# Optimization experiments

Hardware: AMD Instinct MI355X
Metric: run time of the kernel (lower is better)

The kernel has to match this reference:

```python
import jax, jax.numpy as jnp
import numpy as np

MAX_LEN = 200
MAX_K = 3
ITERATION = 3
NEG_PAD = -2.0 ** 16 + 1.0


def setup_inputs() -> dict:
    key = jax.random.key(0)
    k1, k2, k3, k4 = jax.random.split(key, 4)
    B, L, D_in, D_out = 1024, MAX_LEN, 128, 128
    low_capsule = jax.random.normal(k1, (B, L, D_in), dtype=jnp.float32)
    B_matrix = jax.random.normal(k2, (1, MAX_K, L), dtype=jnp.float32)
    S_matrix = jax.random.normal(k3, (D_in, D_out), dtype=jnp.float32)
    # lengths in [1, MAX_LEN]; at least one row hits MAX_LEN so max(seq_len)==MAX_LEN
    seq_len = jax.random.randint(k4, (B, 1), 1, MAX_LEN + 1, dtype=jnp.int64)
    seq_len = seq_len.at[0, 0].set(MAX_LEN)
    return {"low_capsule": low_capsule, "B_matrix": B_matrix,
            "S_matrix": S_matrix, "seq_len": seq_len}


def squash(x):
    # torch code: norm over dim=1 (the capsule axis), keepdim
    sq = jnp.sum(jnp.square(x), axis=1, keepdims=True)
    scale = sq / (1.0 + sq) / jnp.sqrt(sq + 1e-9)
    return scale * x


def reference(low_capsule, B_matrix, S_matrix, seq_len):
    # low_capsule: [B, L, D_in], B_matrix: [1, K, L], S_matrix: [D_in, D_out], seq_len: [B, 1]
    # mask: [B, K, L] (seq_len tiled over K via broadcasting)
    mask = jnp.arange(MAX_LEN)[None, None, :] < seq_len[:, :, None]
    # bilinear projection is loop-invariant (same math as recomputing each iter)
    low_new = jnp.einsum('bld,de->ble', low_capsule, S_matrix)  # [B, L, D_out]
    high = None
    for _ in range(ITERATION):
        logits = jnp.where(mask, B_matrix, jnp.float32(NEG_PAD))  # [B, K, L]
        W = jax.nn.softmax(logits, axis=-1)
        high = squash(jnp.einsum('bkl,ble->bke', W, low_new))  # [B, K, D_out]
        # agreement, summed over batch with keepdim -> [1, K, L]
        B_delta = jnp.einsum('bke,ble->kl', high, low_new)[None]
        B_matrix = B_matrix + B_delta
    return high
```

## Files before the change

kernel.cpp:

```cpp
#include <hip/hip_runtime.h>
#include <math.h>

#define BATCH 1024
#define SEQ   200
#define DIN   128
#define DOUT  128
#define GSTR  260
#define PSTR  608

typedef __attribute__((ext_vector_type(8))) short short8;
typedef __attribute__((ext_vector_type(4))) float f32x4;

__device__ __forceinline__ void async_copy16(const void* g, void* l) {
    __builtin_amdgcn_global_load_lds((const __attribute__((address_space(1))) void*)g,
                                     (__attribute__((address_space(3))) void*)l,
                                     16, 0, 0);
}

__device__ __forceinline__ unsigned pack_split(float f) {
    unsigned u = __float_as_uint(f);
    unsigned r = u + 0x8000u;
    unsigned hi = r >> 16;
    float hf = __uint_as_float(r & 0xffff0000u);
    unsigned lo = __float_as_uint(f - hf) >> 16;
    return (hi << 16) | lo;
}

__device__ __forceinline__ void split2(float f, short& h, short& l) {
    unsigned u = __float_as_uint(f);
    unsigned r = u + 0x8000u;
    h = (short)(r >> 16);
    float hf = __uint_as_float(r & 0xffff0000u);
    l = (short)(__float_as_uint(f - hf) >> 16);
}

__device__ __forceinline__ float unpk(unsigned u) {
    return __uint_as_float(u & 0xffff0000u) + __uint_as_float(u << 16);
}

__global__ __launch_bounds__(256) void k_presplit(const float* __restrict__ S,
                                                  short* __restrict__ Sp) {
    int g = blockIdx.x * 256 + threadIdx.x;
    int j = g & 7, lane = (g >> 3) & 63, kt = (g >> 9) & 3, nt = g >> 11;
    int k = kt * 32 + (lane >> 4) * 8 + j;
    int n = nt * 16 + (lane & 15);
    short h, l;
    split2(S[k * DOUT + n], h, l);
    Sp[g] = h;
    Sp[16384 + g] = l;
}

__global__ __launch_bounds__(256, 4) void k_gemm(const float* __restrict__ A,
                                                 const short* __restrict__ Sp,
                                                 unsigned* __restrict__ outp) {
    __shared__ short sSp[16384];
    const int t = threadIdx.x;
    const int w = t >> 6, lane = t & 63;
    const int q = lane >> 4, c = lane & 15;
    const int cg = blockIdx.x & 1;
    const long rowb = (long)(blockIdx.x >> 1) * 128 + w * 32;

    {
        const int g = w * 4;
#pragma unroll
        for (int i = 0; i < 4; ++i) {
            async_copy16(Sp + cg * 8192 + (g + i) * 512 + lane * 8,
                         &sSp[(g + i) * 512]);
            async_copy16(Sp + 16384 + cg * 8192 + (g + i) * 512 + lane * 8,
                         &sSp[8192 + (g + i) * 512]);
        }
    }

    f32x4 acc[2][4];
    const f32x4 zz = {0.f, 0.f, 0.f, 0.f};
#pragma unroll
    for (int mt = 0; mt < 2; ++mt)
#pragma unroll
        for (int nt = 0; nt < 4; ++nt) acc[mt][nt] = zz;

    float4 buf[2][2][2];
    auto LOADKT = [&](int kt, int p) {
#pragma unroll
        for (int mt = 0; mt < 2; ++mt) {
            const float* ap = A + (rowb + mt * 16 + c) * DIN + kt * 32 + q * 8;
            buf[p][mt][0] = *(const float4*)ap;
            buf[p][mt][1] = *(const float4*)(ap + 4);
        }
    };
    LOADKT(0, 0);
    LOADKT(1, 1);
    __syncthreads();

#pragma unroll
    for (int kt = 0; kt < 4; ++kt) {
        const int p = kt & 1;
        short8 ah[2], al[2];
#pragma unroll
        for (int mt = 0; mt < 2; ++mt) {
            float av[8];
            *(float4*)&av[0] = buf[p][mt][0];
            *(float4*)&av[4] = buf[p][mt][1];
#pragma unroll
            for (int j = 0; j < 8; ++j) {
                short h, l;
                split2(av[j], h, l);
                ah[mt][j] = h; al[mt][j] = l;
            }
        }
        if (kt < 2) LOADKT(kt + 2, p);
#pragma unroll
        for (int nt = 0; nt < 4; ++nt) {
            const int fo = ((nt * 4 + kt) * 64 + lane) * 8;
            short8 sh = *(const short8*)&sSp[fo];
            short8 sl = *(const short8*)&sSp[8192 + fo];
#pragma unroll
            for (int mt = 0; mt < 2; ++mt) {
                acc[mt][nt] = __builtin_amdgcn_mfma_f32_16x16x32_bf16(ah[mt], sh, acc[mt][nt], 0, 0, 0);
                acc[mt][nt] = __builtin_amdgcn_mfma_f32_16x16x32_bf16(al[mt], sh, acc[mt][nt], 0, 0, 0);
                acc[mt][nt] = __builtin_amdgcn_mfma_f32_16x16x32_bf16(ah[mt], sl, acc[mt][nt], 0, 0, 0);
            }
        }
    }
#pragma unroll
    for (int mt = 0; mt < 2; ++mt)
#pragma unroll
        for (int nt = 0; nt < 4; ++nt) {
            const long r0 = rowb + mt * 16 + q * 4;
            const int col = cg * 64 + nt * 16 + c;
#pragma unroll
            for (int r = 0; r < 4; ++r)
                outp[(r0 + r) * DOUT + col] = pack_split(acc[mt][nt][r]);
        }
}

__global__ __launch_bounds__(256, 5) void k_iter(
    const unsigned* __restrict__ lowp,
    const float* __restrict__ Bm,
    const int* __restrict__ seq,
    const float* __restrict__ acc0, const float* __restrict__ acc1,
    float* __restrict__ part,
    float* __restrict__ out, int iter) {
    __shared__ unsigned sLn[25 * GSTR];
    __shared__ float sW[SEQ * 4];
    __shared__ float pB[4][3][32];
    __shared__ float sH[3][32];

    const int t = threadIdx.x, lane = t & 63, w = t >> 6;
    const int b = blockIdx.x >> 2, qr = blockIdx.x & 3;
    const unsigned* lp = lowp + (size_t)b * (SEQ * DIN) + qr * 32;

    float r0[4], r1[4], r2[4];
    if (w < 3) {
#pragma unroll
        for (int i = 0; i < 4; ++i) {
            int l = lane + 64 * i; bool inb = l < SEQ;
            r0[i] = inb ? Bm[w * SEQ + l] : 0.f;
            r1[i] = (inb && iter >= 1) ? acc0[w * SEQ + l] : 0.f;
            r2[i] = (inb && iter >= 2) ? acc1[w * SEQ + l] : 0.f;
        }
    }

    for (int g = w; g < 25; g += 4)
        async_copy16(lp + (g * 8 + (lane >> 3)) * DIN + (lane & 7) * 4,
                     &sLn[g * GSTR]);

    if (w < 3) {
        const int n = seq[b];
        float m = -INFINITY, vv[4];
#pragma unroll
        for (int i = 0; i < 4; ++i) {
            int l = lane + 64 * i;
            float v = r0[i] + r1[i] + r2[i];
            vv[i] = (l < n) ? v : -INFINITY;
            if (l < n) m = fmaxf(m, v);
        }
        for (int off = 32; off; off >>= 1) m = fmaxf(m, __shfl_xor(m, off, 64));
        float s = 0.f, pv[4];
#pragma unroll
        for (int i = 0; i < 4; ++i) {
            pv[i] = (vv[i] == -INFINITY) ? 0.f : expf(vv[i] - m);
            s += pv[i];
        }
        for (int off = 32; off; off >>= 1) s += __shfl_xor(s, off, 64);
        float rs = 1.f / s;
#pragma unroll
        for (int i = 0; i < 4; ++i) {
            int l = lane + 64 * i;
            if (l < SEQ) sW[l * 4 + w] = pv[i] * rs;
        }
    }
    __syncthreads();

    {
        const int el = t & 31, lg = t >> 5;
        float h0 = 0.f, h1 = 0.f, h2 = 0.f;
#pragma unroll
        for (int i = 0; i < 25; ++i) {
            int l = lg * 25 + i;
            float4 wv = *(const float4*)&sW[l * 4];
            float f = unpk(sLn[(l >> 3) * GSTR + (l & 7) * 32 + el]);
            h0 = fmaf(wv.x, f, h0); h1 = fmaf(wv.y, f, h1); h2 = fmaf(wv.z, f, h2);
        }
        h0 += __shfl_xor(h0, 32, 64);
        h1 += __shfl_xor(h1, 32, 64);
        h2 += __shfl_xor(h2, 32, 64);
        if (lane < 32) { pB[w][0][el] = h0; pB[w][1][el] = h1; pB[w][2][el] = h2; }
    }
    __syncthreads();

    if (t < 32) {
        float g0 = pB[0][0][t] + pB[1][0][t] + pB[2][0][t] + pB[3][0][t];
        float g1 = pB[0][1][t] + pB[1][1][t] + pB[2][1][t] + pB[3][1][t];
        float g2 = pB[0][2][t] + pB[1][2][t] + pB[2][2][t] + pB[3][2][t];
        float sq = g0 * g0 + g1 * g1 + g2 * g2;
        float scale = sq / (1.f + sq) / sqrtf(sq + 1e-9f);
        g0 *= scale; g1 *= scale; g2 *= scale;
        if (iter == 2) {
            size_t o = (size_t)b * 3 * DOUT + qr * 32 + t;
            out[o] = g0; out[o + DOUT] = g1; out[o + 2 * DOUT] = g2;
        } else { sH[0][t] = g0; sH[1][t] = g1; sH[2][t] = g2; }
    }
    if (iter == 2) return;
    __syncthreads();

    if (t < SEQ) {
        const int l = t;
        float d0 = 0.f, d1 = 0.f, d2 = 0.f;
#pragma unroll
        for (int j = 0; j < 8; ++j) {
            const int jj = (j + (l & 7) + (l >> 3)) & 7;
            uint4 u = *(const uint4*)&sLn[(l >> 3) * GSTR + (l & 7) * 32 + 4 * jj];
            float4 x0 = *(const float4*)&sH[0][4 * jj];
            float4 x1 = *(const float4*)&sH[1][4 * jj];
            float4 x2 = *(const float4*)&sH[2][4 * jj];
            float f0 = unpk(u.x), f1 = unpk(u.y), f2 = unpk(u.z), f3 = unpk(u.w);
            d0 += x0.x * f0 + x0.y * f1 + x0.z * f2 + x0.w * f3;
            d1 += x1.x * f0 + x1.y * f1 + x1.z * f2 + x1.w * f3;
            d2 += x2.x * f0 + x2.y * f1 + x2.z * f2 + x2.w * f3;
        }
        float* pp = part + (size_t)blockIdx.x * PSTR;
        pp[l] = d0; pp[SEQ + l] = d1; pp[2 * SEQ + l] = d2;
    }
}

__global__ __launch_bounds__(256) void k_reduce(const float* __restrict__ part,
                                                float* __restrict__ accN) {
    const int t = threadIdx.x;
    const int r0 = blockIdx.x * 32;
    if (t < 150) {
        float sx = 0.f, sy = 0.f, sz = 0.f, sw = 0.f;
        for (int r = 0; r < 32; ++r) {
            float4 v = *(const float4*)&part[(size_t)(r0 + r) * PSTR + t * 4];
            sx += v.x; sy += v.y; sz += v.z; sw += v.w;
        }
        atomicAdd(&accN[4 * t + 0], sx);
        atomicAdd(&accN[4 * t + 1], sy);
        atomicAdd(&accN[4 * t + 2], sz);
        atomicAdd(&accN[4 * t + 3], sw);
    }
}

extern "C" void kernel_launch(void* const* d_in, const int* in_sizes, int n_in,
                              void* d_out, int out_size, void* d_ws, size_t ws_size,
                              hipStream_t stream) {
    const float* low_capsule = (const float*)d_in[0];
    const float* B_matrix    = (const float*)d_in[1];
    const float* S_matrix    = (const float*)d_in[2];
    const int*   seq_len     = (const int*)d_in[3];
    float* out = (float*)d_out;

    unsigned* lowp = (unsigned*)d_ws;
    short* Sp      = (short*)(lowp + (size_t)BATCH * SEQ * DOUT);
    float* acc0    = (float*)(Sp + 32768);
    float* acc1    = acc0 + 640;
    float* part    = acc1 + 640;

    hipMemsetAsync(acc0, 0, 1280 * sizeof(float), stream);

    k_presplit<<<64, 256, 0, stream>>>(S_matrix, Sp);
    k_gemm<<<2 * (BATCH * SEQ) / 128, 256, 0, stream>>>(low_capsule, Sp, lowp);

    k_iter<<<4096, 256, 0, stream>>>(lowp, B_matrix, seq_len, acc0, acc1, part, out, 0);
    k_reduce<<<128, 256, 0, stream>>>(part, acc0);
    k_iter<<<4096, 256, 0, stream>>>(lowp, B_matrix, seq_len, acc0, acc1, part, out, 1);
    k_reduce<<<128, 256, 0, stream>>>(part, acc1);
    k_iter<<<4096, 256, 0, stream>>>(lowp, B_matrix, seq_len, acc0, acc1, part, out, 2);
}
```

Baseline: 285.5 us.

## Store projected capsules as plain fp32 and restructure routing kernel to register-resident tiles

The GEMM now writes the projected capsules as ordinary fp32 instead of packed bf16 hi/lo pairs, and it loads all A tiles up front before splitting them. The routing kernel changes from four blocks per batch row staging 32 columns in LDS to two blocks per row. Each thread keeps a 13×float4 slice of the 64 columns in registers, so the softmax, weighted sum and agreement dot products all reuse that data without an LDS staging copy. The agreement reduction now uses wave shuffles, and k_reduce sums 16 partial rows per block. The trade-offs are more register pressure, extra shuffle work, and fewer blocks per kernel launch.

```diff
diff --git a/kernel.cpp b/kernel.cpp
--- a/kernel.cpp
+++ b/kernel.cpp
@@ -5,7 +5,6 @@
 #define SEQ   200
 #define DIN   128
 #define DOUT  128
-#define GSTR  260
 #define PSTR  608
 
 typedef __attribute__((ext_vector_type(8))) short short8;
@@ -15,15 +14,6 @@
     __builtin_amdgcn_global_load_lds((const __attribute__((address_space(1))) void*)g,
                                      (__attribute__((address_space(3))) void*)l,
                                      16, 0, 0);
-}
-
-__device__ __forceinline__ unsigned pack_split(float f) {
-    unsigned u = __float_as_uint(f);
-    unsigned r = u + 0x8000u;
-    unsigned hi = r >> 16;
-    float hf = __uint_as_float(r & 0xffff0000u);
-    unsigned lo = __float_as_uint(f - hf) >> 16;
-    return (hi << 16) | lo;
 }
 
 __device__ __forceinline__ void split2(float f, short& h, short& l) {
@@ -32,10 +22,6 @@
     h = (short)(r >> 16);
     float hf = __uint_as_float(r & 0xffff0000u);
     l = (short)(__float_as_uint(f - hf) >> 16);
-}
-
-__device__ __forceinline__ float unpk(unsigned u) {
-    return __uint_as_float(u & 0xffff0000u) + __uint_as_float(u << 16);
 }
 
 __global__ __launch_bounds__(256) void k_presplit(const float* __restrict__ S,
@@ -52,7 +38,7 @@
 
 __global__ __launch_bounds__(256, 4) void k_gemm(const float* __restrict__ A,
                                                  const short* __restrict__ Sp,
-                                                 unsigned* __restrict__ outp) {
+                                                 float* __restrict__ outn) {
     __shared__ short sSp[16384];
     const int t = threadIdx.x;
     const int w = t >> 6, lane = t & 63;
@@ -60,54 +46,50 @@
     const int cg = blockIdx.x & 1;
     const long rowb = (long)(blockIdx.x >> 1) * 128 + w * 32;
 
-    {
-        const int g = w * 4;
-#pragma unroll
-        for (int i = 0; i < 4; ++i) {
-            async_copy16(Sp + cg * 8192 + (g + i) * 512 + lane * 8,
-                         &sSp[(g + i) * 512]);
-            async_copy16(Sp + 16384 + cg * 8192 + (g + i) * 512 + lane * 8,
-                         &sSp[8192 + (g + i) * 512]);
-        }
-    }
-
-    f32x4 acc[2][4];
-    const f32x4 zz = {0.f, 0.f, 0.f, 0.f};
-#pragma unroll
-    for (int mt = 0; mt < 2; ++mt)
-#pragma unroll
-        for (int nt = 0; nt < 4; ++nt) acc[mt][nt] = zz;
-
-    float4 buf[2][2][2];
-    auto LOADKT = [&](int kt, int p) {
+    float4 araw[4][2][2];
+#pragma unroll
+    for (int kt = 0; kt < 4; ++kt)
 #pragma unroll
         for (int mt = 0; mt < 2; ++mt) {
             const float* ap = A + (rowb + mt * 16 + c) * DIN + kt * 32 + q * 8;
-            buf[p][mt][0] = *(const float4*)ap;
-            buf[p][mt][1] = *(const float4*)(ap + 4);
-        }
-    };
-    LOADKT(0, 0);
-    LOADKT(1, 1);
-    __syncthreads();
-
-#pragma unroll
-    for (int kt = 0; kt < 4; ++kt) {
-        const int p = kt & 1;
-        short8 ah[2], al[2];
+            araw[kt][mt][0] = *(const float4*)ap;
+            araw[kt][mt][1] = *(const float4*)(ap + 4);
+        }
+
+#pragma unroll
+    for (int i = 0; i < 4; ++i) {
+        const int g = w * 4 + i;
+        async_copy16(Sp + cg * 8192 + g * 512 + lane * 8, &sSp[g * 512]);
+        async_copy16(Sp + 16384 + cg * 8192 + g * 512 + lane * 8, &sSp[8192 + g * 512]);
+    }
+
+    short8 ah[4][2], al[4][2];
+#pragma unroll
+    for (int kt = 0; kt < 4; ++kt)
 #pragma unroll
         for (int mt = 0; mt < 2; ++mt) {
             float av[8];
-            *(float4*)&av[0] = buf[p][mt][0];
-            *(float4*)&av[4] = buf[p][mt][1];
+            *(float4*)&av[0] = araw[kt][mt][0];
+            *(float4*)&av[4] = araw[kt][mt][1];
 #pragma unroll
             for (int j = 0; j < 8; ++j) {
                 short h, l;
                 split2(av[j], h, l);
-                ah[mt][j] = h; al[mt][j] = l;
-            }
-        }
-        if (kt < 2) LOADKT(kt + 2, p);
+                ah[kt][mt][j] = h; al[kt][mt][j] = l;
+            }
+        }
+
+    f32x4 acc[2][4];
+    const f32x4 zz = {0.f, 0.f, 0.f, 0.f};
+#pragma unroll
+    for (int mt = 0; mt < 2; ++mt)
+#pragma unroll
+        for (int nt = 0; nt < 4; ++nt) acc[mt][nt] = zz;
+
+    __syncthreads();
+
+#pragma unroll
+    for (int kt = 0; kt < 4; ++kt)
 #pragma unroll
         for (int nt = 0; nt < 4; ++nt) {
             const int fo = ((nt * 4 + kt) * 64 + lane) * 8;
@@ -115,12 +97,11 @@
             short8 sl = *(const short8*)&sSp[8192 + fo];
 #pragma unroll
             for (int mt = 0; mt < 2; ++mt) {
-                acc[mt][nt] = __builtin_amdgcn_mfma_f32_16x16x32_bf16(ah[mt], sh, acc[mt][nt], 0, 0, 0);
-                acc[mt][nt] = __builtin_amdgcn_mfma_f32_16x16x32_bf16(al[mt], sh, acc[mt][nt], 0, 0, 0);
-                acc[mt][nt] = __builtin_amdgcn_mfma_f32_16x16x32_bf16(ah[mt], sl, acc[mt][nt], 0, 0, 0);
-            }
-        }
-    }
+                acc[mt][nt] = __builtin_amdgcn_mfma_f32_16x16x32_bf16(ah[kt][mt], sh, acc[mt][nt], 0, 0, 0);
+                acc[mt][nt] = __builtin_amdgcn_mfma_f32_16x16x32_bf16(al[kt][mt], sh, acc[mt][nt], 0, 0, 0);
+                acc[mt][nt] = __builtin_amdgcn_mfma_f32_16x16x32_bf16(ah[kt][mt], sl, acc[mt][nt], 0, 0, 0);
+            }
+        }
 #pragma unroll
     for (int mt = 0; mt < 2; ++mt)
 #pragma unroll
@@ -129,127 +110,137 @@
             const int col = cg * 64 + nt * 16 + c;
 #pragma unroll
             for (int r = 0; r < 4; ++r)
-                outp[(r0 + r) * DOUT + col] = pack_split(acc[mt][nt][r]);
-        }
-}
-
-__global__ __launch_bounds__(256, 5) void k_iter(
-    const unsigned* __restrict__ lowp,
+                outn[(r0 + r) * DOUT + col] = acc[mt][nt][r];
+        }
+}
+
+__global__ __launch_bounds__(256, 4) void k_iter(
+    const float* __restrict__ lown,
     const float* __restrict__ Bm,
     const int* __restrict__ seq,
     const float* __restrict__ acc0, const float* __restrict__ acc1,
     float* __restrict__ part,
     float* __restrict__ out, int iter) {
-    __shared__ unsigned sLn[25 * GSTR];
-    __shared__ float sW[SEQ * 4];
-    __shared__ float pB[4][3][32];
-    __shared__ float sH[3][32];
-
-    const int t = threadIdx.x, lane = t & 63, w = t >> 6;
-    const int b = blockIdx.x >> 2, qr = blockIdx.x & 3;
-    const unsigned* lp = lowp + (size_t)b * (SEQ * DIN) + qr * 32;
-
-    float r0[4], r1[4], r2[4];
-    if (w < 3) {
-#pragma unroll
-        for (int i = 0; i < 4; ++i) {
-            int l = lane + 64 * i; bool inb = l < SEQ;
-            r0[i] = inb ? Bm[w * SEQ + l] : 0.f;
-            r1[i] = (inb && iter >= 1) ? acc0[w * SEQ + l] : 0.f;
-            r2[i] = (inb && iter >= 2) ? acc1[w * SEQ + l] : 0.f;
-        }
-    }
-
-    for (int g = w; g < 25; g += 4)
-        async_copy16(lp + (g * 8 + (lane >> 3)) * DIN + (lane & 7) * 4,
-                     &sLn[g * GSTR]);
-
-    if (w < 3) {
-        const int n = seq[b];
-        float m = -INFINITY, vv[4];
-#pragma unroll
-        for (int i = 0; i < 4; ++i) {
-            int l = lane + 64 * i;
-            float v = r0[i] + r1[i] + r2[i];
-            vv[i] = (l < n) ? v : -INFINITY;
-            if (l < n) m = fmaxf(m, v);
-        }
-        for (int off = 32; off; off >>= 1) m = fmaxf(m, __shfl_xor(m, off, 64));
+    __shared__ float sW[3][SEQ];
+    __shared__ f32x4 pBf[815];
+    __shared__ float sH[3][64];
+
+    const int t = threadIdx.x, lane = t & 63;
+    const int m = t >> 4, cg = t & 15;
+    const int b = blockIdx.x >> 1, half = blockIdx.x & 1;
+    const float* lp = lown + (size_t)b * (SEQ * DIN) + half * 64;
+
+    float4 dat[13];
+#pragma unroll
+    for (int i = 0; i < 13; ++i) {
+        int r = m + 16 * i;
+        int rc = (r < SEQ) ? r : SEQ - 1;
+        dat[i] = *(const float4*)(lp + rc * DIN + cg * 4);
+    }
+
+    const int n = seq[b];
+#pragma unroll
+    for (int k = 0; k < 3; ++k) {
+        float vv[4], mx = -INFINITY;
+#pragma unroll
+        for (int i2 = 0; i2 < 4; ++i2) {
+            int l = lane + 64 * i2;
+            float v = -INFINITY;
+            if (l < n) {
+                v = Bm[k * SEQ + l];
+                if (iter >= 1) v += acc0[k * SEQ + l];
+                if (iter >= 2) v += acc1[k * SEQ + l];
+            }
+            vv[i2] = v;
+            mx = fmaxf(mx, v);
+        }
+        for (int off = 32; off; off >>= 1) mx = fmaxf(mx, __shfl_xor(mx, off, 64));
         float s = 0.f, pv[4];
 #pragma unroll
-        for (int i = 0; i < 4; ++i) {
-            pv[i] = (vv[i] == -INFINITY) ? 0.f : expf(vv[i] - m);
-            s += pv[i];
+        for (int i2 = 0; i2 < 4; ++i2) {
+            pv[i2] = (vv[i2] == -INFINITY) ? 0.f : expf(vv[i2] - mx);
+            s += pv[i2];
         }
         for (int off = 32; off; off >>= 1) s += __shfl_xor(s, off, 64);
         float rs = 1.f / s;
 #pragma unroll
-        for (int i = 0; i < 4; ++i) {
-            int l = lane + 64 * i;
-            if (l < SEQ) sW[l * 4 + w] = pv[i] * rs;
-        }
-    }
+        for (int i2 = 0; i2 < 4; ++i2) {
+            int l = lane + 64 * i2;
+            if (l < SEQ) sW[k][l] = pv[i2] * rs;
+        }
+    }
+
+    f32x4 h0 = {0.f, 0.f, 0.f, 0.f}, h1 = h0, h2 = h0;
+#pragma unroll
+    for (int i = 0; i < 13; ++i) {
+        int r = m + 16 * i;
+        if (r < SEQ) {
+            float w0 = sW[0][r], w1 = sW[1][r], w2 = sW[2][r];
+            f32x4 f = {dat[i].x, dat[i].y, dat[i].z, dat[i].w};
+            h0 += w0 * f; h1 += w1 * f; h2 += w2 * f;
+        }
+    }
+    pBf[(m * 3 + 0) * 17 + cg] = h0;
+    pBf[(m * 3 + 1) * 17 + cg] = h1;
+    pBf[(m * 3 + 2) * 17 + cg] = h2;
     __syncthreads();
 
-    {
-        const int el = t & 31, lg = t >> 5;
-        float h0 = 0.f, h1 = 0.f, h2 = 0.f;
-#pragma unroll
-        for (int i = 0; i < 25; ++i) {
-            int l = lg * 25 + i;
-            float4 wv = *(const float4*)&sW[l * 4];
-            float f = unpk(sLn[(l >> 3) * GSTR + (l & 7) * 32 + el]);
-            h0 = fmaf(wv.x, f, h0); h1 = fmaf(wv.y, f, h1); h2 = fmaf(wv.z, f, h2);
-        }
-        h0 += __shfl_xor(h0, 32, 64);
-        h1 += __shfl_xor(h1, 32, 64);
-        h2 += __shfl_xor(h2, 32, 64);
-        if (lane < 32) { pB[w][0][el] = h0; pB[w][1][el] = h1; pB[w][2][el] = h2; }
-    }
-    __syncthreads();
-
-    if (t < 32) {
-        float g0 = pB[0][0][t] + pB[1][0][t] + pB[2][0][t] + pB[3][0][t];
-        float g1 = pB[0][1][t] + pB[1][1][t] + pB[2][1][t] + pB[3][1][t];
-        float g2 = pB[0][2][t] + pB[1][2][t] + pB[2][2][t] + pB[3][2][t];
+    if (t < 64) {
+        const int ecg = t >> 2, ej = t & 3;
+        float g0 = 0.f, g1 = 0.f, g2 = 0.f;
+#pragma unroll
+        for (int mm = 0; mm < 16; ++mm) {
+            g0 += pBf[(mm * 3 + 0) * 17 + ecg][ej];
+            g1 += pBf[(mm * 3 + 1) * 17 + ecg][ej];
+            g2 += pBf[(mm * 3 + 2) * 17 + ecg][ej];
+        }
         float sq = g0 * g0 + g1 * g1 + g2 * g2;
         float scale = sq / (1.f + sq) / sqrtf(sq + 1e-9f);
         g0 *= scale; g1 *= scale; g2 *= scale;
         if (iter == 2) {
-            size_t o = (size_t)b * 3 * DOUT + qr * 32 + t;
+            size_t o = (size_t)b * 3 * DOUT + half * 64 + t;
             out[o] = g0; out[o + DOUT] = g1; out[o + 2 * DOUT] = g2;
-        } else { sH[0][t] = g0; sH[1][t] = g1; sH[2][t] = g2; }
+        } else {
+            sH[0][t] = g0; sH[1][t] = g1; sH[2][t] = g2;
+        }
     }
     if (iter == 2) return;
     __syncthreads();
 
-    if (t < SEQ) {
-        const int l = t;
-        float d0 = 0.f, d1 = 0.f, d2 = 0.f;
-#pragma unroll
-        for (int j = 0; j < 8; ++j) {
-            const int jj = (j + (l & 7) + (l >> 3)) & 7;
-            uint4 u = *(const uint4*)&sLn[(l >> 3) * GSTR + (l & 7) * 32 + 4 * jj];
-            float4 x0 = *(const float4*)&sH[0][4 * jj];
-            float4 x1 = *(const float4*)&sH[1][4 * jj];
-            float4 x2 = *(const float4*)&sH[2][4 * jj];
-            float f0 = unpk(u.x), f1 = unpk(u.y), f2 = unpk(u.z), f3 = unpk(u.w);
-            d0 += x0.x * f0 + x0.y * f1 + x0.z * f2 + x0.w * f3;
-            d1 += x1.x * f0 + x1.y * f1 + x1.z * f2 + x1.w * f3;
-            d2 += x2.x * f0 + x2.y * f1 + x2.z * f2 + x2.w * f3;
-        }
-        float* pp = part + (size_t)blockIdx.x * PSTR;
-        pp[l] = d0; pp[SEQ + l] = d1; pp[2 * SEQ + l] = d2;
+    f32x4 x0 = *(const f32x4*)&sH[0][cg * 4];
+    f32x4 x1 = *(const f32x4*)&sH[1][cg * 4];
+    f32x4 x2 = *(const f32x4*)&sH[2][cg * 4];
+    float* pp = part + (size_t)blockIdx.x * PSTR;
+#pragma unroll
+    for (int i = 0; i < 13; ++i) {
+        int r = m + 16 * i;
+        if (r < SEQ) {
+            f32x4 f = {dat[i].x, dat[i].y, dat[i].z, dat[i].w};
+            f32x4 p0 = x0 * f, p1 = x1 * f, p2 = x2 * f;
+            float d0 = p0[0] + p0[1] + p0[2] + p0[3];
+            float d1 = p1[0] + p1[1] + p1[2] + p1[3];
+            float d2 = p2[0] + p2[1] + p2[2] + p2[3];
+#pragma unroll
+            for (int off = 1; off < 16; off <<= 1) {
+                d0 += __shfl_xor(d0, off, 64);
+                d1 += __shfl_xor(d1, off, 64);
+                d2 += __shfl_xor(d2, off, 64);
+            }
+            if (cg == 0) {
+                pp[r] = d0; pp[SEQ + r] = d1; pp[2 * SEQ + r] = d2;
+            }
+        }
     }
 }
 
 __global__ __launch_bounds__(256) void k_reduce(const float* __restrict__ part,
                                                 float* __restrict__ accN) {
     const int t = threadIdx.x;
-    const int r0 = blockIdx.x * 32;
+    const int r0 = blockIdx.x * 16;
     if (t < 150) {
         float sx = 0.f, sy = 0.f, sz = 0.f, sw = 0.f;
-        for (int r = 0; r < 32; ++r) {
+#pragma unroll
+        for (int r = 0; r < 16; ++r) {
             float4 v = *(const float4*)&part[(size_t)(r0 + r) * PSTR + t * 4];
             sx += v.x; sy += v.y; sz += v.z; sw += v.w;
         }
@@ -269,20 +260,20 @@
     const int*   seq_len     = (const int*)d_in[3];
     float* out = (float*)d_out;
 
-    unsigned* lowp = (unsigned*)d_ws;
-    short* Sp      = (short*)(lowp + (size_t)BATCH * SEQ * DOUT);
-    float* acc0    = (float*)(Sp + 32768);
-    float* acc1    = acc0 + 640;
-    float* part    = acc1 + 640;
+    float* lown = (float*)d_ws;
+    short* Sp   = (short*)(lown + (size_t)BATCH * SEQ * DOUT);
+    float* acc0 = (float*)(Sp + 32768);
+    float* acc1 = acc0 + 640;
+    float* part = acc1 + 640;
 
     hipMemsetAsync(acc0, 0, 1280 * sizeof(float), stream);
 
     k_presplit<<<64, 256, 0, stream>>>(S_matrix, Sp);
-    k_gemm<<<2 * (BATCH * SEQ) / 128, 256, 0, stream>>>(low_capsule, Sp, lowp);
-
-    k_iter<<<4096, 256, 0, stream>>>(lowp, B_matrix, seq_len, acc0, acc1, part, out, 0);
+    k_gemm<<<2 * (BATCH * SEQ) / 128, 256, 0, stream>>>(low_capsule, Sp, lown);
+
+    k_iter<<<2 * BATCH, 256, 0, stream>>>(lown, B_matrix, seq_len, acc0, acc1, part, out, 0);
     k_reduce<<<128, 256, 0, stream>>>(part, acc0);
-    k_iter<<<4096, 256, 0, stream>>>(lowp, B_matrix, seq_len, acc0, acc1, part, out, 1);
+    k_iter<<<2 * BATCH, 256, 0, stream>>>(lown, B_matrix, seq_len, acc0, acc1, part, out, 1);
     k_reduce<<<128, 256, 0, stream>>>(part, acc1);
-    k_iter<<<4096, 256, 0, stream>>>(lowp, B_matrix, seq_len, acc0, acc1, part, out, 2);
-}
+    k_iter<<<2 * BATCH, 256, 0, stream>>>(lown, B_matrix, seq_len, acc0, acc1, part, out, 2);
+}
```

Result: slower. 293.2 us (+2.7%).
